# Kernel optimization log

Measured on AMD Instinct MI355X. Metric: run time of the kernel, lower is better.

## Reference

```python
import jax, jax.numpy as jnp
import numpy as np

B, C, IMG = 512, 3, 112


def setup_inputs() -> dict:
    key = jax.random.key(0)
    k0, k1, k2 = jax.random.split(key, 3)
    img = jax.random.normal(k0, (B, C, IMG, IMG), dtype=jnp.float32)
    # fc[0]: Linear(3*H*W -> 20); fc[3]: Linear(20 -> 6) init weight=0, bias=identity.
    # Use small random W2 so the warp is non-trivial (math identical regardless).
    W1 = jax.random.normal(k1, (C * IMG * IMG, 20), dtype=jnp.float32) * 0.005
    b1 = jnp.zeros((20,), dtype=jnp.float32)
    W2 = jax.random.normal(k2, (20, 6), dtype=jnp.float32) * 0.01
    b2 = jnp.array([1, 0, 0, 0, 1, 0], dtype=jnp.float32)
    return {"img": img, "W1": W1, "b1": b1, "W2": W2, "b2": b2}


def reference(img, W1, b1, W2, b2):
    Bn, Cn, H, W = img.shape
    h = jnp.tanh(img.reshape(Bn, -1) @ W1 + b1)            # [B, 20]
    theta = jnp.tanh(h @ W2 + b2).reshape(Bn, 2, 3)        # [B, 2, 3]

    # F.affine_grid, align_corners=False: pixel-center normalized coords
    xs = (2.0 * jnp.arange(W, dtype=jnp.float32) + 1.0) / W - 1.0
    ys = (2.0 * jnp.arange(H, dtype=jnp.float32) + 1.0) / H - 1.0
    gy, gx = jnp.meshgrid(ys, xs, indexing="ij")           # [H, W]
    base = jnp.stack([gx, gy, jnp.ones_like(gx)], axis=-1)  # [H, W, 3] -> (x, y, 1)
    grid = jnp.einsum("bij,hwj->bhwi", theta, base)        # [B, H, W, 2], (x, y)

    # F.grid_sample, bilinear, padding_mode='zeros', align_corners=False
    ix = ((grid[..., 0] + 1.0) * W - 1.0) * 0.5            # [B, H, W] src x
    iy = ((grid[..., 1] + 1.0) * H - 1.0) * 0.5            # [B, H, W] src y
    x0f = jnp.floor(ix); y0f = jnp.floor(iy)
    wx1 = ix - x0f; wx0 = 1.0 - wx1
    wy1 = iy - y0f; wy0 = 1.0 - wy1

    img_hwc = img.transpose(0, 2, 3, 1)                    # [B, H, W, C]
    bidx = jnp.arange(Bn)[:, None, None]

    def gather(xf, yf):
        valid = (xf >= 0) & (xf <= W - 1) & (yf >= 0) & (yf <= H - 1)
        xc = jnp.clip(xf, 0, W - 1).astype(jnp.int32)
        yc = jnp.clip(yf, 0, H - 1).astype(jnp.int32)
        v = img_hwc[bidx, yc, xc]                           # [B, H, W, C]
        return v * valid[..., None].astype(img.dtype)

    out = (gather(x0f, y0f) * (wx0 * wy0)[..., None]
           + gather(x0f + 1, y0f) * (wx1 * wy0)[..., None]
           + gather(x0f, y0f + 1) * (wx0 * wy1)[..., None]
           + gather(x0f + 1, y0f + 1) * (wx1 * wy1)[..., None])
    return out.transpose(0, 3, 1, 2)                       # [B, C, H, W]
```

## Files before the change

### kernel.cpp

```cpp
#include <hip/hip_runtime.h>
#include <math.h>

#define BATCH 512
#define CHAN 3
#define IMG 112
#define HW (IMG*IMG)
#define K_TOT (CHAN*HW)
#define NH 20
#define F4_TOT (K_TOT/4)
#define KT 21
#define F4_PER_TILE (F4_TOT/KT)
#define MBB 8
#define NPW 5

__global__ __launch_bounds__(256)
void transpose_w1(const float* __restrict__ W1, float* __restrict__ W1T) {
    const int k = blockIdx.x * 256 + threadIdx.x;
    float4 r[5];
    #pragma unroll
    for (int q = 0; q < 5; ++q)
        r[q] = *reinterpret_cast<const float4*>(W1 + (long)k * NH + q * 4);
    const float* f = reinterpret_cast<const float*>(r);
    #pragma unroll
    for (int n = 0; n < NH; ++n)
        W1T[(long)n * K_TOT + k] = f[n];
}

__global__ __launch_bounds__(256)
void gemm1_kernel(const float* __restrict__ img, const float* __restrict__ W1T,
                  float* __restrict__ partial) {
    const int tid  = threadIdx.x;
    const int wave = tid >> 6, lane = tid & 63;
    const int kt   = blockIdx.x;
    const int b0   = blockIdx.y * MBB;
    const int n0   = wave * NPW;

    float acc[MBB][NPW];
    #pragma unroll
    for (int b = 0; b < MBB; ++b)
        #pragma unroll
        for (int n = 0; n < NPW; ++n) acc[b][n] = 0.f;

    const int f4start = kt * F4_PER_TILE;

    #pragma unroll 1
    for (int it = 0; it < F4_PER_TILE / 64; ++it) {
        const int k = (f4start + it * 64 + lane) * 4;
        float4 wq[NPW];
        float4 iv[MBB];
        #pragma unroll
        for (int n = 0; n < NPW; ++n)
            wq[n] = *reinterpret_cast<const float4*>(W1T + (long)(n0 + n) * K_TOT + k);
        #pragma unroll
        for (int b = 0; b < MBB; ++b)
            iv[b] = *reinterpret_cast<const float4*>(img + (long)(b0 + b) * K_TOT + k);

        #pragma unroll
        for (int b = 0; b < MBB; ++b)
            #pragma unroll
            for (int n = 0; n < NPW; ++n) {
                acc[b][n] = fmaf(iv[b].x, wq[n].x, acc[b][n]);
                acc[b][n] = fmaf(iv[b].y, wq[n].y, acc[b][n]);
                acc[b][n] = fmaf(iv[b].z, wq[n].z, acc[b][n]);
                acc[b][n] = fmaf(iv[b].w, wq[n].w, acc[b][n]);
            }
    }

    __shared__ float red[MBB * NH];
    #pragma unroll
    for (int b = 0; b < MBB; ++b)
        #pragma unroll
        for (int n = 0; n < NPW; ++n) {
            float v = acc[b][n];
            #pragma unroll
            for (int off = 32; off > 0; off >>= 1) v += __shfl_xor(v, off, 64);
            if (lane == 0) red[b * NH + (n0 + n)] = v;
        }
    __syncthreads();
    if (tid < MBB * NH)
        partial[((long)kt * BATCH + b0) * NH + tid] = red[tid];
}

__global__ __launch_bounds__(64)
void theta_kernel(const float* __restrict__ partial, const float* __restrict__ b1,
                  const float* __restrict__ W2, const float* __restrict__ b2,
                  float* __restrict__ theta) {
    const int b = blockIdx.x;
    const int t = threadIdx.x;
    __shared__ float h[NH];
    if (t < NH) {
        float s = b1[t];
        #pragma unroll
        for (int kt = 0; kt < KT; ++kt)
            s += partial[((long)kt * BATCH + b) * NH + t];
        h[t] = tanhf(s);
    }
    __syncthreads();
    if (t < 6) {
        float s = b2[t];
        #pragma unroll
        for (int n = 0; n < NH; ++n) s = fmaf(h[n], W2[n * 6 + t], s);
        theta[b * 6 + t] = tanhf(s);
    }
}

#define QUADS (HW/4)
__global__ __launch_bounds__(256)
void warp_kernel(const float* __restrict__ img, const float* __restrict__ theta,
                 float* __restrict__ out) {
    const int b = blockIdx.y;
    const int quad = blockIdx.x * 256 + threadIdx.x;
    if (quad >= QUADS) return;
    const int y  = quad / (IMG / 4);
    const int x0 = (quad - y * (IMG / 4)) * 4;

    const float* t = theta + b * 6;
    const float t0 = t[0], t1 = t[1], t2 = t[2], t3 = t[3], t4 = t[4], t5 = t[5];
    const float ys = (2.f * y + 1.f) / (float)IMG - 1.f;

    const long ib = (long)b * CHAN * HW;
    float res[CHAN][4];

    #pragma unroll
    for (int i = 0; i < 4; ++i) {
        const float xs = (2.f * (x0 + i) + 1.f) / (float)IMG - 1.f;
        const float gx = t0 * xs + t1 * ys + t2;
        const float gy = t3 * xs + t4 * ys + t5;

        const float ix = ((gx + 1.f) * (float)IMG - 1.f) * 0.5f;
        const float iy = ((gy + 1.f) * (float)IMG - 1.f) * 0.5f;

        const float x0f = floorf(ix), y0f = floorf(iy);
        const float wx1 = ix - x0f, wx0 = 1.f - wx1;
        const float wy1 = iy - y0f, wy0 = 1.f - wy1;
        const int sx0 = (int)x0f, sy0 = (int)y0f;
        const int sx1 = sx0 + 1, sy1 = sy0 + 1;

        const bool vx0 = (sx0 >= 0) & (sx0 <= IMG - 1);
        const bool vx1 = (sx1 >= 0) & (sx1 <= IMG - 1);
        const bool vy0 = (sy0 >= 0) & (sy0 <= IMG - 1);
        const bool vy1 = (sy1 >= 0) & (sy1 <= IMG - 1);
        const int cx0 = min(max(sx0, 0), IMG - 1), cx1 = min(max(sx1, 0), IMG - 1);
        const int cy0 = min(max(sy0, 0), IMG - 1), cy1 = min(max(sy1, 0), IMG - 1);

        const float w00 = (vx0 && vy0) ? wx0 * wy0 : 0.f;
        const float w10 = (vx1 && vy0) ? wx1 * wy0 : 0.f;
        const float w01 = (vx0 && vy1) ? wx0 * wy1 : 0.f;
        const float w11 = (vx1 && vy1) ? wx1 * wy1 : 0.f;

        const int o00 = cy0 * IMG + cx0, o10 = cy0 * IMG + cx1;
        const int o01 = cy1 * IMG + cx0, o11 = cy1 * IMG + cx1;
        #pragma unroll
        for (int c = 0; c < CHAN; ++c) {
            const float* p = img + ib + (long)c * HW;
            res[c][i] = w00 * p[o00] + w10 * p[o10] + w01 * p[o01] + w11 * p[o11];
        }
    }

    const int pix0 = y * IMG + x0;
    #pragma unroll
    for (int c = 0; c < CHAN; ++c) {
        float4 v = make_float4(res[c][0], res[c][1], res[c][2], res[c][3]);
        *reinterpret_cast<float4*>(out + ib + (long)c * HW + pix0) = v;
    }
}

extern "C" void kernel_launch(void* const* d_in, const int* in_sizes, int n_in,
                              void* d_out, int out_size, void* d_ws, size_t ws_size,
                              hipStream_t stream) {
    const float* img = (const float*)d_in[0];
    const float* W1  = (const float*)d_in[1];
    const float* b1  = (const float*)d_in[2];
    const float* W2  = (const float*)d_in[3];
    const float* b2  = (const float*)d_in[4];
    float* out = (float*)d_out;

    float* partial = (float*)d_ws;
    float* theta   = partial + (long)KT * BATCH * NH;
    float* W1T     = theta + BATCH * 6;

    transpose_w1<<<dim3(K_TOT / 256), 256, 0, stream>>>(W1, W1T);
    gemm1_kernel<<<dim3(KT, BATCH / MBB), 256, 0, stream>>>(img, W1T, partial);
    theta_kernel<<<dim3(BATCH), 64, 0, stream>>>(partial, b1, W2, b2, theta);
    warp_kernel<<<dim3((QUADS + 255) / 256, BATCH), 256, 0, stream>>>(img, theta, out);
}
```

Before: 225.4 us.

## Stage image planes in LDS for warp and double-buffer GEMM loads

```diff
diff --git a/kernel.cpp b/kernel.cpp
--- a/kernel.cpp
+++ b/kernel.cpp
@@ -10,6 +10,7 @@
 #define F4_TOT (K_TOT/4)
 #define KT 21
 #define F4_PER_TILE (F4_TOT/KT)
+#define ITERS (F4_PER_TILE/64)
 #define MBB 8
 #define NPW 5
 
@@ -34,6 +35,7 @@
     const int kt   = blockIdx.x;
     const int b0   = blockIdx.y * MBB;
     const int n0   = wave * NPW;
+    const int f4start = kt * F4_PER_TILE;
 
     float acc[MBB][NPW];
     #pragma unroll
@@ -41,30 +43,41 @@
         #pragma unroll
         for (int n = 0; n < NPW; ++n) acc[b][n] = 0.f;
 
-    const int f4start = kt * F4_PER_TILE;
-
+    float4 wqA[NPW], ivA[MBB], wqB[NPW], ivB[MBB];
+
+#define LOADS(WQ, IV, IT)                                                        \
+    {                                                                            \
+        const int k_ = (f4start + (IT) * 64 + lane) * 4;                         \
+        _Pragma("unroll")                                                        \
+        for (int n = 0; n < NPW; ++n)                                            \
+            WQ[n] = *reinterpret_cast<const float4*>(W1T + (long)(n0 + n) * K_TOT + k_); \
+        _Pragma("unroll")                                                        \
+        for (int b = 0; b < MBB; ++b)                                            \
+            IV[b] = *reinterpret_cast<const float4*>(img + (long)(b0 + b) * K_TOT + k_); \
+    }
+
+#define FMAS(WQ, IV)                                                             \
+    {                                                                            \
+        _Pragma("unroll")                                                        \
+        for (int b = 0; b < MBB; ++b)                                            \
+            _Pragma("unroll")                                                    \
+            for (int n = 0; n < NPW; ++n) {                                      \
+                acc[b][n] = fmaf(IV[b].x, WQ[n].x, acc[b][n]);                   \
+                acc[b][n] = fmaf(IV[b].y, WQ[n].y, acc[b][n]);                   \
+                acc[b][n] = fmaf(IV[b].z, WQ[n].z, acc[b][n]);                   \
+                acc[b][n] = fmaf(IV[b].w, WQ[n].w, acc[b][n]);                   \
+            }                                                                    \
+    }
+
+    LOADS(wqA, ivA, 0);
     #pragma unroll 1
-    for (int it = 0; it < F4_PER_TILE / 64; ++it) {
-        const int k = (f4start + it * 64 + lane) * 4;
-        float4 wq[NPW];
-        float4 iv[MBB];
-        #pragma unroll
-        for (int n = 0; n < NPW; ++n)
-            wq[n] = *reinterpret_cast<const float4*>(W1T + (long)(n0 + n) * K_TOT + k);
-        #pragma unroll
-        for (int b = 0; b < MBB; ++b)
-            iv[b] = *reinterpret_cast<const float4*>(img + (long)(b0 + b) * K_TOT + k);
-
-        #pragma unroll
-        for (int b = 0; b < MBB; ++b)
-            #pragma unroll
-            for (int n = 0; n < NPW; ++n) {
-                acc[b][n] = fmaf(iv[b].x, wq[n].x, acc[b][n]);
-                acc[b][n] = fmaf(iv[b].y, wq[n].y, acc[b][n]);
-                acc[b][n] = fmaf(iv[b].z, wq[n].z, acc[b][n]);
-                acc[b][n] = fmaf(iv[b].w, wq[n].w, acc[b][n]);
-            }
-    }
+    for (int it = 0; it < ITERS - 1; it += 2) {
+        LOADS(wqB, ivB, it + 1);
+        FMAS(wqA, ivA);
+        LOADS(wqA, ivA, it + 2);
+        FMAS(wqB, ivB);
+    }
+    FMAS(wqA, ivA);
 
     __shared__ float red[MBB * NH];
     #pragma unroll
@@ -108,60 +121,62 @@
 __global__ __launch_bounds__(256)
 void warp_kernel(const float* __restrict__ img, const float* __restrict__ theta,
                  float* __restrict__ out) {
-    const int b = blockIdx.y;
-    const int quad = blockIdx.x * 256 + threadIdx.x;
-    if (quad >= QUADS) return;
-    const int y  = quad / (IMG / 4);
-    const int x0 = (quad - y * (IMG / 4)) * 4;
+    const int b = blockIdx.x;
+    const int c = blockIdx.y;
+    const long ibc = ((long)b * CHAN + c) * HW;
+
+    __shared__ float tile[HW];
+    for (int i = threadIdx.x; i < HW / 4; i += 256)
+        reinterpret_cast<float4*>(tile)[i] =
+            reinterpret_cast<const float4*>(img + ibc)[i];
 
     const float* t = theta + b * 6;
     const float t0 = t[0], t1 = t[1], t2 = t[2], t3 = t[3], t4 = t[4], t5 = t[5];
-    const float ys = (2.f * y + 1.f) / (float)IMG - 1.f;
-
-    const long ib = (long)b * CHAN * HW;
-    float res[CHAN][4];
-
-    #pragma unroll
-    for (int i = 0; i < 4; ++i) {
-        const float xs = (2.f * (x0 + i) + 1.f) / (float)IMG - 1.f;
-        const float gx = t0 * xs + t1 * ys + t2;
-        const float gy = t3 * xs + t4 * ys + t5;
-
-        const float ix = ((gx + 1.f) * (float)IMG - 1.f) * 0.5f;
-        const float iy = ((gy + 1.f) * (float)IMG - 1.f) * 0.5f;
-
-        const float x0f = floorf(ix), y0f = floorf(iy);
-        const float wx1 = ix - x0f, wx0 = 1.f - wx1;
-        const float wy1 = iy - y0f, wy0 = 1.f - wy1;
-        const int sx0 = (int)x0f, sy0 = (int)y0f;
-        const int sx1 = sx0 + 1, sy1 = sy0 + 1;
-
-        const bool vx0 = (sx0 >= 0) & (sx0 <= IMG - 1);
-        const bool vx1 = (sx1 >= 0) & (sx1 <= IMG - 1);
-        const bool vy0 = (sy0 >= 0) & (sy0 <= IMG - 1);
-        const bool vy1 = (sy1 >= 0) & (sy1 <= IMG - 1);
-        const int cx0 = min(max(sx0, 0), IMG - 1), cx1 = min(max(sx1, 0), IMG - 1);
-        const int cy0 = min(max(sy0, 0), IMG - 1), cy1 = min(max(sy1, 0), IMG - 1);
-
-        const float w00 = (vx0 && vy0) ? wx0 * wy0 : 0.f;
-        const float w10 = (vx1 && vy0) ? wx1 * wy0 : 0.f;
-        const float w01 = (vx0 && vy1) ? wx0 * wy1 : 0.f;
-        const float w11 = (vx1 && vy1) ? wx1 * wy1 : 0.f;
-
-        const int o00 = cy0 * IMG + cx0, o10 = cy0 * IMG + cx1;
-        const int o01 = cy1 * IMG + cx0, o11 = cy1 * IMG + cx1;
-        #pragma unroll
-        for (int c = 0; c < CHAN; ++c) {
-            const float* p = img + ib + (long)c * HW;
-            res[c][i] = w00 * p[o00] + w10 * p[o10] + w01 * p[o01] + w11 * p[o11];
+    __syncthreads();
+
+    #pragma unroll 1
+    for (int q = threadIdx.x; q < QUADS; q += 256) {
+        const int y  = q / (IMG / 4);
+        const int x0 = (q - y * (IMG / 4)) * 4;
+        const float ys = (2.f * y + 1.f) / (float)IMG - 1.f;
+        float res[4];
+
+        #pragma unroll
+        for (int i = 0; i < 4; ++i) {
+            const float xs = (2.f * (x0 + i) + 1.f) / (float)IMG - 1.f;
+            const float gx = t0 * xs + t1 * ys + t2;
+            const float gy = t3 * xs + t4 * ys + t5;
+
+            const float ix = ((gx + 1.f) * (float)IMG - 1.f) * 0.5f;
+            const float iy = ((gy + 1.f) * (float)IMG - 1.f) * 0.5f;
+
+            const float x0f = floorf(ix), y0f = floorf(iy);
+            const float wx1 = ix - x0f, wx0 = 1.f - wx1;
+            const float wy1 = iy - y0f, wy0 = 1.f - wy1;
+            const int sx0 = (int)x0f, sy0 = (int)y0f;
+            const int sx1 = sx0 + 1, sy1 = sy0 + 1;
+
+            const bool vx0 = (sx0 >= 0) & (sx0 <= IMG - 1);
+            const bool vx1 = (sx1 >= 0) & (sx1 <= IMG - 1);
+            const bool vy0 = (sy0 >= 0) & (sy0 <= IMG - 1);
+            const bool vy1 = (sy1 >= 0) & (sy1 <= IMG - 1);
+            const int cx0 = min(max(sx0, 0), IMG - 1), cx1 = min(max(sx1, 0), IMG - 1);
+            const int cy0 = min(max(sy0, 0), IMG - 1), cy1 = min(max(sy1, 0), IMG - 1);
+
+            const float w00 = (vx0 && vy0) ? wx0 * wy0 : 0.f;
+            const float w10 = (vx1 && vy0) ? wx1 * wy0 : 0.f;
+            const float w01 = (vx0 && vy1) ? wx0 * wy1 : 0.f;
+            const float w11 = (vx1 && vy1) ? wx1 * wy1 : 0.f;
+
+            const float v00 = tile[cy0 * IMG + cx0];
+            const float v10 = tile[cy0 * IMG + cx1];
+            const float v01 = tile[cy1 * IMG + cx0];
+            const float v11 = tile[cy1 * IMG + cx1];
+            res[i] = w00 * v00 + w10 * v10 + w01 * v01 + w11 * v11;
         }
-    }
-
-    const int pix0 = y * IMG + x0;
-    #pragma unroll
-    for (int c = 0; c < CHAN; ++c) {
-        float4 v = make_float4(res[c][0], res[c][1], res[c][2], res[c][3]);
-        *reinterpret_cast<float4*>(out + ib + (long)c * HW + pix0) = v;
+
+        *reinterpret_cast<float4*>(out + ibc + y * IMG + x0) =
+            make_float4(res[0], res[1], res[2], res[3]);
     }
 }
 
@@ -182,5 +197,5 @@
     transpose_w1<<<dim3(K_TOT / 256), 256, 0, stream>>>(W1, W1T);
     gemm1_kernel<<<dim3(KT, BATCH / MBB), 256, 0, stream>>>(img, W1T, partial);
     theta_kernel<<<dim3(BATCH), 64, 0, stream>>>(partial, b1, W2, b2, theta);
-    warp_kernel<<<dim3((QUADS + 255) / 256, BATCH), 256, 0, stream>>>(img, theta, out);
-}
+    warp_kernel<<<dim3(BATCH, CHAN), 256, 0, stream>>>(img, theta, out);
+}
```

Result: faster. 202.2 us (-10.3%).
